# Performance work log

Measured on AMD Instinct MI355X. Metric: run time of the kernel, lower is better.

Reference implementation:

```python
import jax, jax.numpy as jnp
import numpy as np

B, T = 2, 2048
D_MODEL = 1024
N_LAYERS = 2
VOCAB = 256
BLOCK = 2048
LOCAL = 128
STRIDE = 256
NHEAD = D_MODEL // 64  # 16
HEAD_DIM = D_MODEL // NHEAD  # 64
LN_EPS = 1e-5


def setup_inputs() -> dict:
    key = jax.random.key(0)
    ks = jax.random.split(key, 16)
    L, d = N_LAYERS, D_MODEL

    def g(k, shape, scale=0.02):
        return (jax.random.normal(k, shape, dtype=jnp.float32) * scale)

    return {
        "x": jax.random.randint(ks[0], (B, T), 0, VOCAB),
        "embed": g(ks[1], (VOCAB, d)),
        "pos_embed": g(ks[2], (BLOCK, d)),
        # per-layer weights stacked on leading L axis; Linear as y = x @ W + b
        "Wq": g(ks[3], (L, d, d)), "bq": jnp.zeros((L, d), jnp.float32),
        "Wk": g(ks[4], (L, d, d)), "bk": jnp.zeros((L, d), jnp.float32),
        "Wv": g(ks[5], (L, d, d)), "bv": jnp.zeros((L, d), jnp.float32),
        "Wo": g(ks[6], (L, d, d)), "bo": jnp.zeros((L, d), jnp.float32),
        "g1": jnp.ones((L, d), jnp.float32), "be1": jnp.zeros((L, d), jnp.float32),
        "W1": g(ks[7], (L, d, 4 * d)), "bf1": jnp.zeros((L, 4 * d), jnp.float32),
        "W2": g(ks[8], (L, 4 * d, d)), "bf2": jnp.zeros((L, d), jnp.float32),
        "g2": jnp.ones((L, d), jnp.float32), "be2": jnp.zeros((L, d), jnp.float32),
        "gf": jnp.ones((d,), jnp.float32), "bef": jnp.zeros((d,), jnp.float32),
        "Whead": g(ks[9], (d, VOCAB)),
    }


def _ln(x, gamma, beta):
    mu = jnp.mean(x, axis=-1, keepdims=True)
    var = jnp.mean(jnp.square(x - mu), axis=-1, keepdims=True)
    return (x - mu) * jax.lax.rsqrt(var + LN_EPS) * gamma + beta


def _sparse_mask(t):
    # allowed[i, j] = True if token i may attend to token j
    i = jnp.arange(t)[:, None]
    j = jnp.arange(t)[None, :]
    causal = j <= i
    local = (i - j) <= LOCAL
    glob = (j % STRIDE) == 0
    return causal & (local | glob)


def _sparse_attn(q, k, v, allowed):
    # q, k, v: [B, T, D] -> [B, H, T, hd]
    b, t, d = q.shape
    def split(x):
        return x.reshape(b, t, NHEAD, HEAD_DIM).transpose(0, 2, 1, 3)
    q, k, v = split(q), split(k), split(v)
    scale = HEAD_DIM ** -0.5
    scores = jnp.einsum("bhqd,bhkd->bhqk", q, k) * scale
    scores = jnp.where(allowed[None, None], scores, -jnp.inf)
    attn = jax.nn.softmax(scores, axis=-1)  # every row has j=i allowed -> no NaN
    out = jnp.einsum("bhqk,bhkd->bhqd", attn, v)
    return out.transpose(0, 2, 1, 3).reshape(b, t, d)


def reference(x, embed, pos_embed, Wq, bq, Wk, bk, Wv, bv, Wo, bo,
              g1, be1, W1, bf1, W2, bf2, g2, be2, gf, bef, Whead):
    b, t = x.shape
    h = embed[x] + pos_embed[jnp.arange(t)][None]
    allowed = _sparse_mask(t)
    for l in range(N_LAYERS):
        h_n = _ln(h, g1[l], be1[l])
        q = h_n @ Wq[l] + bq[l]
        k = h_n @ Wk[l] + bk[l]
        v = h_n @ Wv[l] + bv[l]
        attn_out = _sparse_attn(q, k, v, allowed)
        h = h + (attn_out @ Wo[l] + bo[l])
        h2 = _ln(h, g2[l], be2[l])
        ffn = jax.nn.gelu(h2 @ W1[l] + bf1[l], approximate=False) @ W2[l] + bf2[l]
        h = h + ffn
    h = _ln(h, gf, bef)
    return h @ Whead
```

## Files before the change

### kernel.cpp

```cpp
#include <hip/hip_runtime.h>
#include <hip/hip_bf16.h>

#define BB 2
#define TT 2048
#define DD 1024
#define FF 4096
#define VV 256
#define HH 16
#define HD 64
#define MM (BB * TT)
#define LOCAL_W 128
#define STRIDE_G 256
#define QS 3072

typedef short s16x8 __attribute__((ext_vector_type(8)));
typedef __bf16 bf16x8 __attribute__((ext_vector_type(8)));
typedef float f32x4 __attribute__((ext_vector_type(4)));

#define WAITVM(N) asm volatile("s_waitcnt vmcnt(" #N ")" ::: "memory")
#define CFENCE asm volatile("" ::: "memory")

__device__ __forceinline__ float b2f(unsigned short u) {
  return __builtin_bit_cast(float, (unsigned int)u << 16);
}
__device__ __forceinline__ unsigned short f2b(float f) {
  __hip_bfloat16 h = __float2bfloat16(f);
  return __builtin_bit_cast(unsigned short, h);
}
__device__ __forceinline__ void gl_lds16(const unsigned short* g, unsigned short* l) {
  __builtin_amdgcn_global_load_lds(
      (const __attribute__((address_space(1))) void*)g,
      (__attribute__((address_space(3))) void*)l, 16, 0, 0);
}
__device__ __forceinline__ bf16x8 ldsr(const unsigned short* p) {
  return __builtin_bit_cast(bf16x8, *(const s16x8*)p);
}

__global__ __launch_bounds__(256) void transpose_k(const float* __restrict__ W,
                                                   unsigned short* __restrict__ WT,
                                                   int K, int N,
                                                   size_t sstride, size_t dstride) {
  __shared__ float t[32][33];
  const int z = blockIdx.z;
  W += (size_t)z * sstride;
  WT += (size_t)z * dstride;
  const int n0 = blockIdx.x * 32, k0 = blockIdx.y * 32;
  const int tx = threadIdx.x, ty = threadIdx.y;
  for (int r = ty; r < 32; r += 8) t[r][tx] = W[(size_t)(k0 + r) * N + n0 + tx];
  __syncthreads();
  for (int r = ty; r < 32; r += 8)
    WT[(size_t)(n0 + r) * K + k0 + tx] = f2b(t[tx][r]);
}

__global__ __launch_bounds__(256) void qkv_t(const float* __restrict__ Wq,
                                             const float* __restrict__ Wk,
                                             const float* __restrict__ Wv,
                                             unsigned short* __restrict__ WT) {
  __shared__ float t[32][33];
  const int z = blockIdx.z;
  const int l = z / 3, which = z % 3;
  const float* W = (which == 0 ? Wq : which == 1 ? Wk : Wv) + (size_t)l * DD * DD;
  unsigned short* D = WT + ((size_t)l * QS + which * DD) * DD;
  const int n0 = blockIdx.x * 32, k0 = blockIdx.y * 32;
  const int tx = threadIdx.x, ty = threadIdx.y;
  for (int r = ty; r < 32; r += 8) t[r][tx] = W[(size_t)(k0 + r) * DD + n0 + tx];
  __syncthreads();
  for (int r = ty; r < 32; r += 8)
    D[(size_t)(n0 + r) * DD + k0 + tx] = f2b(t[tx][r]);
}

__global__ __launch_bounds__(256) void concat_bias(const float* __restrict__ bq,
                                                   const float* __restrict__ bk,
                                                   const float* __restrict__ bv,
                                                   float* __restrict__ bcat) {
  const int i = blockIdx.x * 256 + threadIdx.x;
  const int l = i / QS, j = i - l * QS;
  float v;
  if (j < DD) v = bq[l * DD + j];
  else if (j < 2 * DD) v = bk[l * DD + j - DD];
  else v = bv[l * DD + j - 2 * DD];
  bcat[i] = v;
}

__global__ __launch_bounds__(256) void embed_ln(const int* __restrict__ x,
                                                const float* __restrict__ emb,
                                                const float* __restrict__ pos,
                                                const float* __restrict__ g,
                                                const float* __restrict__ be,
                                                float* __restrict__ h,
                                                unsigned short* __restrict__ out) {
  const int row = blockIdx.x;
  const int tid = threadIdx.x;
  const int tok = x[row];
  const int t = row & (TT - 1);
  f32x4 v = *(const f32x4*)&emb[(size_t)tok * DD + tid * 4];
  v += *(const f32x4*)&pos[(size_t)t * DD + tid * 4];
  *(f32x4*)&h[(size_t)row * DD + tid * 4] = v;
  float s = v[0] + v[1] + v[2] + v[3];
  float sq = v[0] * v[0] + v[1] * v[1] + v[2] * v[2] + v[3] * v[3];
#pragma unroll
  for (int off = 32; off; off >>= 1) {
    s += __shfl_xor(s, off);
    sq += __shfl_xor(sq, off);
  }
  __shared__ float ss[4], ssq[4];
  const int w = tid >> 6, lane = tid & 63;
  if (lane == 0) { ss[w] = s; ssq[w] = sq; }
  __syncthreads();
  s = ss[0] + ss[1] + ss[2] + ss[3];
  sq = ssq[0] + ssq[1] + ssq[2] + ssq[3];
  const float mean = s * (1.0f / DD);
  const float var = sq * (1.0f / DD) - mean * mean;
  const float rstd = rsqrtf(var + 1e-5f);
  const float4 gv = *(const float4*)&g[tid * 4];
  const float4 bv = *(const float4*)&be[tid * 4];
  ushort4 o;
  o.x = f2b((v[0] - mean) * rstd * gv.x + bv.x);
  o.y = f2b((v[1] - mean) * rstd * gv.y + bv.y);
  o.z = f2b((v[2] - mean) * rstd * gv.z + bv.z);
  o.w = f2b((v[3] - mean) * rstd * gv.w + bv.w);
  *(ushort4*)&out[(size_t)row * DD + tid * 4] = o;
}

__global__ __launch_bounds__(256) void ln_red(float* __restrict__ hio,
                                              const float* __restrict__ parts,
                                              const float* __restrict__ bias,
                                              const float* __restrict__ g,
                                              const float* __restrict__ be,
                                              unsigned short* __restrict__ out) {
  const int row = blockIdx.x;
  const int tid = threadIdx.x;
  const size_t base = (size_t)row * DD + tid * 4;
  f32x4 v = *(const f32x4*)&hio[base];
  v += *(const f32x4*)&bias[tid * 4];
  v += *(const f32x4*)&parts[base];
  v += *(const f32x4*)&parts[(size_t)MM * DD + base];
  *(f32x4*)&hio[base] = v;
  float s = v[0] + v[1] + v[2] + v[3];
  float sq = v[0] * v[0] + v[1] * v[1] + v[2] * v[2] + v[3] * v[3];
#pragma unroll
  for (int off = 32; off; off >>= 1) {
    s += __shfl_xor(s, off);
    sq += __shfl_xor(sq, off);
  }
  __shared__ float ss[4], ssq[4];
  const int w = tid >> 6, lane = tid & 63;
  if (lane == 0) { ss[w] = s; ssq[w] = sq; }
  __syncthreads();
  s = ss[0] + ss[1] + ss[2] + ss[3];
  sq = ssq[0] + ssq[1] + ssq[2] + ssq[3];
  const float mean = s * (1.0f / DD);
  const float var = sq * (1.0f / DD) - mean * mean;
  const float rstd = rsqrtf(var + 1e-5f);
  const float4 gv = *(const float4*)&g[tid * 4];
  const float4 bv = *(const float4*)&be[tid * 4];
  ushort4 o;
  o.x = f2b((v[0] - mean) * rstd * gv.x + bv.x);
  o.y = f2b((v[1] - mean) * rstd * gv.y + bv.y);
  o.z = f2b((v[2] - mean) * rstd * gv.z + bv.z);
  o.w = f2b((v[3] - mean) * rstd * gv.w + bv.w);
  *(ushort4*)&out[(size_t)row * DD + tid * 4] = o;
}

template <int EPI>
__global__ __launch_bounds__(512, 2) void gemm8p(const unsigned short* __restrict__ A,
                                                 const unsigned short* __restrict__ BT,
                                                 const float* __restrict__ bias,
                                                 unsigned short* __restrict__ outp,
                                                 int M, int N, int K, int nbx) {
  __shared__ __align__(16) unsigned short lds[65536];
  const int tid = threadIdx.x;
  const int lane = tid & 63;
  const int w = tid >> 6;
  const int nwg = gridDim.x;
  const int orig = blockIdx.x;
  const int wg = (orig & 7) * (nwg >> 3) + (orig >> 3);
  const int n0 = (wg % nbx) * 256, m0 = (wg / nbx) * 256;
  const int wm = w >> 2, wn = w & 3;
  f32x4 acc[8][4] = {};

  const unsigned short* aSrc[2];
  const unsigned short* bSrc[2];
  int dstO[2];
#pragma unroll
  for (int i = 0; i < 2; i++) {
    const int s = tid + (i << 9);
    const int row = s >> 2, sc = s & 3;
    const int l = sc ^ ((row >> 1) & 3);
    aSrc[i] = &A[(size_t)(m0 + row) * K + l * 8];
    bSrc[i] = &BT[(size_t)(n0 + row) * K + l * 8];
    dstO[i] = s * 8;
  }
  auto STAGE = [&](int tb, int ks, int obase) {
    const int kt = (tb << 6) + (ks << 5);
    const int so = obase + ks * 16384;
#pragma unroll
    for (int i = 0; i < 2; i++) {
      gl_lds16(aSrc[i] + kt, &lds[so + dstO[i]]);
      gl_lds16(bSrc[i] + kt, &lds[so + 8192 + dstO[i]]);
    }
  };

  const int rA = lane & 15, cr = lane >> 4;
  const int rowA0 = wm * 128 + rA;
  const int rowB0 = wn * 64 + rA;
  const int aAddr0 = rowA0 * 32 + ((cr ^ ((rowA0 >> 1) & 3)) << 3);
  const int bAddr0 = 8192 + rowB0 * 32 + ((cr ^ ((rowB0 >> 1) & 3)) << 3);

  const int NT = K >> 6;
  STAGE(0, 0, 0);
  STAGE(0, 1, 0);

  auto TILE = [&](int bufc, int tb, bool notlast) {
    const int bb = bufc << 15;
    const int ob = (bufc ^ 1) << 15;
    bf16x8 bfr[4], af[4];
    WAITVM(4);
    __builtin_amdgcn_s_barrier();
    CFENCE;
    if (notlast) STAGE(tb + 1, 0, ob);
#pragma unroll
    for (int n = 0; n < 4; n++) bfr[n] = ldsr(&lds[bb + bAddr0 + n * 512]);
#pragma unroll
    for (int i = 0; i < 4; i++) af[i] = ldsr(&lds[bb + aAddr0 + i * 512]);
    __builtin_amdgcn_s_setprio(1);
#pragma unroll
    for (int i = 0; i < 4; i++)
#pragma unroll
      for (int n = 0; n < 4; n++)
        acc[i][n] = __builtin_amdgcn_mfma_f32_16x16x32_bf16(af[i], bfr[n], acc[i][n], 0, 0, 0);
    __builtin_amdgcn_s_setprio(0);
#pragma unroll
    for (int i = 0; i < 4; i++) af[i] = ldsr(&lds[bb + aAddr0 + (4 + i) * 512]);
    __builtin_amdgcn_s_setprio(1);
#pragma unroll
    for (int i = 0; i < 4; i++)
#pragma unroll
      for (int n = 0; n < 4; n++)
        acc[4 + i][n] = __builtin_amdgcn_mfma_f32_16x16x32_bf16(af[i], bfr[n], acc[4 + i][n], 0, 0, 0);
    __builtin_amdgcn_s_setprio(0);
    if (notlast) { WAITVM(4); } else { WAITVM(0); }
    __builtin_amdgcn_s_barrier();
    CFENCE;
    if (notlast) STAGE(tb + 1, 1, ob);
#pragma unroll
    for (int n = 0; n < 4; n++) bfr[n] = ldsr(&lds[bb + 16384 + bAddr0 + n * 512]);
#pragma unroll
    for (int i = 0; i < 4; i++) af[i] = ldsr(&lds[bb + 16384 + aAddr0 + i * 512]);
    __builtin_amdgcn_s_setprio(1);
#pragma unroll
    for (int i = 0; i < 4; i++)
#pragma unroll
      for (int n = 0; n < 4; n++)
        acc[i][n] = __builtin_amdgcn_mfma_f32_16x16x32_bf16(af[i], bfr[n], acc[i][n], 0, 0, 0);
    __builtin_amdgcn_s_setprio(0);
#pragma unroll
    for (int i = 0; i < 4; i++) af[i] = ldsr(&lds[bb + 16384 + aAddr0 + (4 + i) * 512]);
    __builtin_amdgcn_s_setprio(1);
#pragma unroll
    for (int i = 0; i < 4; i++)
#pragma unroll
      for (int n = 0; n < 4; n++)
        acc[4 + i][n] = __builtin_amdgcn_mfma_f32_16x16x32_bf16(af[i], bfr[n], acc[4 + i][n], 0, 0, 0);
    __builtin_amdgcn_s_setprio(0);
  };

  for (int it = 0; it < NT; it += 2) {
    TILE(0, it, true);
    TILE(1, it + 1, it + 2 < NT);
  }

  const int r0 = (lane >> 4) * 4;
  const int cc = lane & 15;
#pragma unroll
  for (int m = 0; m < 8; m++) {
#pragma unroll
    for (int n = 0; n < 4; n++) {
#pragma unroll
      for (int r = 0; r < 4; r++) {
        const int row = m0 + wm * 128 + m * 16 + r0 + r;
        const int col = n0 + wn * 64 + n * 16 + cc;
        float val = acc[m][n][r] + bias[col];
        if (EPI == 3) {
          float u = val * (0.7978845608f + 0.0356774081f * val * val);
          u = fminf(u, 10.0f);
          const float e = __expf(2.0f * u);
          val = val * e / (e + 1.0f);
        }
        outp[(size_t)row * N + col] = f2b(val);
      }
    }
  }
}

template <int EPI>
__global__ __launch_bounds__(512, 2) void gemm_dw(const unsigned short* __restrict__ A,
                                                  const unsigned short* __restrict__ BT,
                                                  const float* __restrict__ bias,
                                                  void* __restrict__ outp,
                                                  int M, int N, int K, int nbx, int nwg2,
                                                  int ksub) {
  __shared__ __align__(16) unsigned short lds[49152];
  const int tid = threadIdx.x;
  const int lane = tid & 63;
  const int w = tid >> 6;
  const int nwg = gridDim.x;
  const int orig = blockIdx.x;
  const int wg = (orig & 7) * (nwg >> 3) + (orig >> 3);
  const int ks = wg / nwg2;
  const int rem = wg - ks * nwg2;
  const int n0 = (rem % nbx) * 128;
  const int m0 = (rem / nbx) * 256;
  const int kb = ks * ksub;
  const int wm = w >> 2, wn = w & 3;
  f32x4 acc[8][2] = {};

  const unsigned short* aSrc[2];
  const unsigned short* bSrc;
  int dstA[2], dstB;
#pragma unroll
  for (int i = 0; i < 2; i++) {
    const int s = tid + (i << 9);
    const int row = s >> 2, sc = s & 3;
    const int l = sc ^ ((row >> 1) & 3);
    aSrc[i] = &A[(size_t)(m0 + row) * K + kb + l * 8];
    dstA[i] = s * 8;
  }
  {
    const int row = tid >> 2, sc = tid & 3;
    const int l = sc ^ ((row >> 1) & 3);
    bSrc = &BT[(size_t)(n0 + row) * K + kb + l * 8];
    dstB = 8192 + tid * 8;
  }
  auto STAGE = [&](int tb, int kss, int obase) {
    const int kt = (tb << 6) + (kss << 5);
    const int so = obase + kss * 12288;
    gl_lds16(aSrc[0] + kt, &lds[so + dstA[0]]);
    gl_lds16(aSrc[1] + kt, &lds[so + dstA[1]]);
    gl_lds16(bSrc + kt, &lds[so + dstB]);
  };

  const int rA = lane & 15, cr = lane >> 4;
  const int rowA0 = wm * 128 + rA;
  const int rowB0 = wn * 32 + rA;
  const int aAddr0 = rowA0 * 32 + ((cr ^ ((rowA0 >> 1) & 3)) << 3);
  const int bAddr0 = 8192 + rowB0 * 32 + ((cr ^ ((rowB0 >> 1) & 3)) << 3);

  const int NT = ksub >> 6;
  STAGE(0, 0, 0);
  STAGE(0, 1, 0);

  auto TILE = [&](int bufc, int tb, bool notlast) {
    const int bb = bufc * 24576;
    const int ob = (bufc ^ 1) * 24576;
    bf16x8 bfr[2], af[4];
    WAITVM(3);
    __builtin_amdgcn_s_barrier();
    CFENCE;
    if (notlast) STAGE(tb + 1, 0, ob);
#pragma unroll
    for (int n = 0; n < 2; n++) bfr[n] = ldsr(&lds[bb + bAddr0 + n * 512]);
#pragma unroll
    for (int i = 0; i < 4; i++) af[i] = ldsr(&lds[bb + aAddr0 + i * 512]);
    __builtin_amdgcn_s_setprio(1);
#pragma unroll
    for (int i = 0; i < 4; i++)
#pragma unroll
      for (int n = 0; n < 2; n++)
        acc[i][n] = __builtin_amdgcn_mfma_f32_16x16x32_bf16(af[i], bfr[n], acc[i][n], 0, 0, 0);
    __builtin_amdgcn_s_setprio(0);
#pragma unroll
    for (int i = 0; i < 4; i++) af[i] = ldsr(&lds[bb + aAddr0 + (4 + i) * 512]);
    __builtin_amdgcn_s_setprio(1);
#pragma unroll
    for (int i = 0; i < 4; i++)
#pragma unroll
      for (int n = 0; n < 2; n++)
        acc[4 + i][n] = __builtin_amdgcn_mfma_f32_16x16x32_bf16(af[i], bfr[n], acc[4 + i][n], 0, 0, 0);
    __builtin_amdgcn_s_setprio(0);
    if (notlast) { WAITVM(3); } else { WAITVM(0); }
    __builtin_amdgcn_s_barrier();
    CFENCE;
    if (notlast) STAGE(tb + 1, 1, ob);
#pragma unroll
    for (int n = 0; n < 2; n++) bfr[n] = ldsr(&lds[bb + 12288 + bAddr0 + n * 512]);
#pragma unroll
    for (int i = 0; i < 4; i++) af[i] = ldsr(&lds[bb + 12288 + aAddr0 + i * 512]);
    __builtin_amdgcn_s_setprio(1);
#pragma unroll
    for (int i = 0; i < 4; i++)
#pragma unroll
      for (int n = 0; n < 2; n++)
        acc[i][n] = __builtin_amdgcn_mfma_f32_16x16x32_bf16(af[i], bfr[n], acc[i][n], 0, 0, 0);
    __builtin_amdgcn_s_setprio(0);
#pragma unroll
    for (int i = 0; i < 4; i++) af[i] = ldsr(&lds[bb + 12288 + aAddr0 + (4 + i) * 512]);
    __builtin_amdgcn_s_setprio(1);
#pragma unroll
    for (int i = 0; i < 4; i++)
#pragma unroll
      for (int n = 0; n < 2; n++)
        acc[4 + i][n] = __builtin_amdgcn_mfma_f32_16x16x32_bf16(af[i], bfr[n], acc[4 + i][n], 0, 0, 0);
    __builtin_amdgcn_s_setprio(0);
  };

  for (int it = 0; it < NT; it += 2) {
    TILE(0, it, true);
    TILE(1, it + 1, it + 2 < NT);
  }

  const int r0 = (lane >> 4) * 4;
  const int cc = lane & 15;
#pragma unroll
  for (int m = 0; m < 8; m++)
#pragma unroll
    for (int n = 0; n < 2; n++)
#pragma unroll
      for (int r = 0; r < 4; r++) {
        const int row = m0 + wm * 128 + m * 16 + r0 + r;
        const int col = n0 + wn * 32 + n * 16 + cc;
        const size_t idx = (size_t)row * N + col;
        if (EPI == 0) {
          ((float*)outp)[(size_t)ks * M * N + idx] = acc[m][n][r];
        } else {
          ((unsigned short*)outp)[idx] = f2b(acc[m][n][r] + bias[col]);
        }
      }
}

__global__ __launch_bounds__(512, 2) void gemm_p(const unsigned short* __restrict__ A,
                                                 const unsigned short* __restrict__ BT,
                                                 float* __restrict__ outp,
                                                 int M, int N, int K, int nbx, int nwg2,
                                                 int ksub) {
  constexpr int BM = 128;
  __shared__ __align__(16) unsigned short lds[4][BM * 64];
  const int tid = threadIdx.x;
  const int lane = tid & 63;
  const int w = tid >> 6;
  const int nwg = gridDim.x;
  const int orig = blockIdx.x;
  const int wg = (orig & 7) * (nwg >> 3) + (orig >> 3);
  const int ks = wg / nwg2;
  const int rem = wg - ks * nwg2;
  const int n0 = (rem % nbx) * BM;
  const int m0 = (rem / nbx) * BM;
  const int kb = ks * ksub;
  const int wm = w >> 2, wn = w & 3;
  f32x4 acc[4][2] = {};

  auto STAGE = [&](int t) {
    const int b = t & 3;
    const int kt = kb + (t << 5);
    const int s = tid;
    const int row = s >> 2, sc = s & 3;
    const int c = sc ^ ((row >> 1) & 3);
    gl_lds16(&A[(size_t)(m0 + row) * K + kt + c * 8], &lds[b][s * 8]);
    gl_lds16(&BT[(size_t)(n0 + row) * K + kt + c * 8], &lds[b][BM * 32 + s * 8]);
  };

  const int NT = ksub >> 5;
  STAGE(0); STAGE(1); STAGE(2);

  for (int t = 0; t < NT; ++t) {
    const int ahead = NT - 1 - t;
    if (ahead >= 2) WAITVM(4); else if (ahead == 1) WAITVM(2); else WAITVM(0);
    __builtin_amdgcn_s_barrier();
    CFENCE;
    if (t + 3 < NT) STAGE(t + 3);
    const int b = t & 3;
    const int rA = lane & 15, cr = lane >> 4;
    bf16x8 af[4], bfr[2];
#pragma unroll
    for (int m = 0; m < 4; m++) {
      const int row = wm * 64 + m * 16 + rA;
      af[m] = ldsr(&lds[b][row * 32 + ((cr ^ ((row >> 1) & 3)) << 3)]);
    }
#pragma unroll
    for (int n = 0; n < 2; n++) {
      const int row = wn * 32 + n * 16 + rA;
      bfr[n] = ldsr(&lds[b][BM * 32 + row * 32 + ((cr ^ ((row >> 1) & 3)) << 3)]);
    }
    __builtin_amdgcn_s_setprio(1);
#pragma unroll
    for (int m = 0; m < 4; m++)
#pragma unroll
      for (int n = 0; n < 2; n++)
        acc[m][n] = __builtin_amdgcn_mfma_f32_16x16x32_bf16(af[m], bfr[n], acc[m][n], 0, 0, 0);
    __builtin_amdgcn_s_setprio(0);
  }

  const int r0 = (lane >> 4) * 4;
  const int cc = lane & 15;
  float* pout = outp + (size_t)ks * M * N;
#pragma unroll
  for (int m = 0; m < 4; m++)
#pragma unroll
    for (int n = 0; n < 2; n++)
#pragma unroll
      for (int r = 0; r < 4; r++) {
        const int row = m0 + wm * 64 + m * 16 + r0 + r;
        const int col = n0 + wn * 32 + n * 16 + cc;
        pout[(size_t)row * N + col] = acc[m][n][r];
      }
}

template <int NP>
__global__ __launch_bounds__(256) void reduce_k(float* __restrict__ dst,
                                                const float* __restrict__ parts,
                                                size_t total) {
  const size_t i = ((size_t)blockIdx.x * 256 + threadIdx.x) * 4;
  if (i >= total) return;
  f32x4 acc = {};
#pragma unroll
  for (int p = 0; p < NP; p++) acc += *(const f32x4*)&parts[(size_t)p * total + i];
  *(f32x4*)&dst[i] = acc;
}

#define QT 16
#define KT 32
#define NTMAX 6
#define KP 72
#define PP 40

__global__ __launch_bounds__(256) void attn_mfma(const unsigned short* __restrict__ qkv,
                                                 unsigned short* __restrict__ outg) {
  __shared__ __align__(16) unsigned short kvs[4][KT * KP];
  __shared__ __align__(16) unsigned short pls[4][QT * PP];
  const int tid = threadIdx.x;
  const int wid = tid >> 6, lane = tid & 63;
  const int qgrp = blockIdx.x & 31;
  const int bh = blockIdx.x >> 5;
  const int h = bh & (HH - 1), b = bh >> 4;
  const size_t baseq = (size_t)b * TT * QS + (size_t)h * HD;
  const size_t baseo = (size_t)b * TT * DD + (size_t)h * HD;
  const int i0 = qgrp * 64 + wid * 16;
  const int g = lane >> 4;
  const int c = lane & 15;

  const int i0b = qgrp * 64 + 48;
  const int ka0b = (i0b > 128) ? ((i0b - 128) & ~31) : 0;
  const int nlb = ((i0b + 16 - ka0b) + 31) >> 5;
  const int neb = (ka0b + 255) >> 8;
  const int ka0 = (i0 > 128) ? ((i0 - 128) & ~31) : 0;
  const int ne = (ka0 + 255) >> 8;

  const s16x8 qf0 = *(const s16x8*)&qkv[baseq + (size_t)(i0 + c) * QS + g * 8];
  const s16x8 qf1 = *(const s16x8*)&qkv[baseq + (size_t)(i0 + c) * QS + 32 + g * 8];

  f32x4 sc[NTMAX][2];
  float smax[4] = {-1e30f, -1e30f, -1e30f, -1e30f};

#pragma unroll
  for (int t = 0; t < NTMAX; t++) {
    if (t > nlb) continue;
    const bool isg = (t == 0);
    if (isg && neb == 0) continue;
    const int kt0 = ka0 + (t - 1) * 32;
#pragma unroll
    for (int it = 0; it < 4; it++) {
      const int row = it * 8 + (lane >> 3);
      const int ch = lane & 7;
      const int j = isg ? ((row < ne) ? row * STRIDE_G : 0) : (kt0 + row);
      *(s16x8*)&kvs[wid][row * KP + ch * 8] =
          *(const s16x8*)&qkv[baseq + DD + (size_t)j * QS + ch * 8];
    }
    __syncthreads();
#pragma unroll
    for (int half = 0; half < 2; half++) {
      const int key = half * 16 + c;
      const bf16x8 kb0 = __builtin_bit_cast(bf16x8, *(const s16x8*)&kvs[wid][key * KP + g * 8]);
      const bf16x8 kb1 = __builtin_bit_cast(bf16x8, *(const s16x8*)&kvs[wid][key * KP + 32 + g * 8]);
      f32x4 a = {};
      a = __builtin_amdgcn_mfma_f32_16x16x32_bf16(__builtin_bit_cast(bf16x8, qf0), kb0, a, 0, 0, 0);
      a = __builtin_amdgcn_mfma_f32_16x16x32_bf16(__builtin_bit_cast(bf16x8, qf1), kb1, a, 0, 0, 0);
#pragma unroll
      for (int r = 0; r < 4; r++) {
        const int i = i0 + g * 4 + r;
        bool ok;
        if (isg) {
          ok = (key < ne);
        } else {
          const int j = kt0 + key;
          ok = (j <= i) && (((i - j) <= LOCAL_W) || ((j & (STRIDE_G - 1)) == 0));
        }
        const float s = ok ? a[r] * 0.125f : -1e30f;
        sc[t][half][r] = s;
        smax[r] = fmaxf(smax[r], s);
      }
    }
    __syncthreads();
  }
#pragma unroll
  for (int r = 0; r < 4; r++)
#pragma unroll
    for (int off = 8; off; off >>= 1)
      smax[r] = fmaxf(smax[r], __shfl_xor(smax[r], off));

  f32x4 o[4] = {};
  float lsum[4] = {0.f, 0.f, 0.f, 0.f};
#pragma unroll
  for (int t = 0; t < NTMAX; t++) {
    if (t > nlb) continue;
    const bool isg = (t == 0);
    if (isg && neb == 0) continue;
    const int kt0 = ka0 + (t - 1) * 32;
#pragma unroll
    for (int it = 0; it < 4; it++) {
      const int row = it * 8 + (lane >> 3);
      const int ch = lane & 7;
      const int j = isg ? ((row < ne) ? row * STRIDE_G : 0) : (kt0 + row);
      *(s16x8*)&kvs[wid][row * KP + ch * 8] =
          *(const s16x8*)&qkv[baseq + 2 * DD + (size_t)j * QS + ch * 8];
    }
#pragma unroll
    for (int half = 0; half < 2; half++)
#pragma unroll
      for (int r = 0; r < 4; r++) {
        const float p = __expf(sc[t][half][r] - smax[r]);
        lsum[r] += p;
        pls[wid][(g * 4 + r) * PP + half * 16 + c] = f2b(p);
      }
    __syncthreads();
    const bf16x8 pa = __builtin_bit_cast(bf16x8, *(const s16x8*)&pls[wid][c * PP + g * 8]);
#pragma unroll
    for (int d0 = 0; d0 < 4; d0++) {
      s16x8 bv;
#pragma unroll
      for (int e = 0; e < 8; e++)
        bv[e] = (short)kvs[wid][(g * 8 + e) * KP + d0 * 16 + c];
      o[d0] = __builtin_amdgcn_mfma_f32_16x16x32_bf16(pa, __builtin_bit_cast(bf16x8, bv), o[d0], 0, 0, 0);
    }
    __syncthreads();
  }
#pragma unroll
  for (int r = 0; r < 4; r++)
#pragma unroll
    for (int off = 8; off; off >>= 1)
      lsum[r] += __shfl_xor(lsum[r], off);
#pragma unroll
  for (int d0 = 0; d0 < 4; d0++)
#pragma unroll
    for (int r = 0; r < 4; r++)
      outg[baseo + (size_t)(i0 + g * 4 + r) * DD + d0 * 16 + c] = f2b(o[d0][r] / lsum[r]);
}

extern "C" void kernel_launch(void* const* d_in, const int* in_sizes, int n_in,
                              void* d_out, int out_size, void* d_ws, size_t ws_size,
                              hipStream_t stream) {
  const int* x = (const int*)d_in[0];
  const float* embed = (const float*)d_in[1];
  const float* pos = (const float*)d_in[2];
  const float* Wq = (const float*)d_in[3];
  const float* bq = (const float*)d_in[4];
  const float* Wk = (const float*)d_in[5];
  const float* bk = (const float*)d_in[6];
  const float* Wv = (const float*)d_in[7];
  const float* bv = (const float*)d_in[8];
  const float* Wo = (const float*)d_in[9];
  const float* bo = (const float*)d_in[10];
  const float* g1 = (const float*)d_in[11];
  const float* be1 = (const float*)d_in[12];
  const float* W1 = (const float*)d_in[13];
  const float* bf1 = (const float*)d_in[14];
  const float* W2 = (const float*)d_in[15];
  const float* bf2 = (const float*)d_in[16];
  const float* g2 = (const float*)d_in[17];
  const float* be2 = (const float*)d_in[18];
  const float* gf = (const float*)d_in[19];
  const float* bef = (const float*)d_in[20];
  const float* Whead = (const float*)d_in[21];

  char* ws = (char*)d_ws;
  size_t off = 0;
  auto alloc = [&](size_t bytes) -> void* {
    void* p = ws + off;
    off += (bytes + 255) & ~(size_t)255;
    return p;
  };
  unsigned short* WqkvT = (unsigned short*)alloc((size_t)2 * QS * DD * 2);
  unsigned short* WoT = (unsigned short*)alloc((size_t)2 * DD * DD * 2);
  unsigned short* W1T = (unsigned short*)alloc((size_t)2 * DD * FF * 2);
  unsigned short* W2T = (unsigned short*)alloc((size_t)2 * DD * FF * 2);
  unsigned short* WheadT = (unsigned short*)alloc((size_t)DD * VV * 2);
  float* bcat = (float*)alloc((size_t)2 * QS * 4);
  float* h = (float*)alloc((size_t)MM * DD * 4);
  unsigned short* hn = (unsigned short*)alloc((size_t)MM * DD * 2);
  unsigned short* qkvb = (unsigned short*)alloc((size_t)MM * QS * 2);
  unsigned short* attnb = (unsigned short*)alloc((size_t)MM * DD * 2);
  unsigned short* mid = (unsigned short*)alloc((size_t)MM * FF * 2);
  float* ffn2p = (float*)qkvb;
  float* oprojp = (float*)mid;
  float* headp = (float*)mid;
  (void)ws_size;

  const dim3 tb(32, 8);
  qkv_t<<<dim3(DD / 32, DD / 32, 6), tb, 0, stream>>>(Wq, Wk, Wv, WqkvT);
  transpose_k<<<dim3(DD / 32, DD / 32, 2), tb, 0, stream>>>(Wo, WoT, DD, DD,
                                                            (size_t)DD * DD, (size_t)DD * DD);
  transpose_k<<<dim3(FF / 32, DD / 32, 2), tb, 0, stream>>>(W1, W1T, DD, FF,
                                                            (size_t)DD * FF, (size_t)DD * FF);
  transpose_k<<<dim3(DD / 32, FF / 32, 2), tb, 0, stream>>>(W2, W2T, FF, DD,
                                                            (size_t)DD * FF, (size_t)DD * FF);
  transpose_k<<<dim3(VV / 32, DD / 32, 1), tb, 0, stream>>>(Whead, WheadT, DD, VV, 0, 0);
  concat_bias<<<24, 256, 0, stream>>>(bq, bk, bv, bcat);

  embed_ln<<<MM, 256, 0, stream>>>(x, embed, pos, g1, be1, h, hn);

  for (int l = 0; l < 2; l++) {
    const size_t wo = (size_t)l * DD * DD;
    const size_t wf = (size_t)l * DD * FF;
    gemm_dw<1><<<(QS / 128) * (MM / 256), 512, 0, stream>>>(
        hn, WqkvT + (size_t)l * QS * DD, bcat + l * QS, qkvb,
        MM, QS, DD, QS / 128, (QS / 128) * (MM / 256), DD);
    attn_mfma<<<BB * HH * (TT / 64), 256, 0, stream>>>(qkvb, attnb);
    gemm_dw<0><<<2 * (DD / 128) * (MM / 256), 512, 0, stream>>>(
        attnb, WoT + wo, nullptr, oprojp,
        MM, DD, DD, DD / 128, (DD / 128) * (MM / 256), DD / 2);
    ln_red<<<MM, 256, 0, stream>>>(h, oprojp, bo + l * DD, g2 + l * DD, be2 + l * DD, hn);
    gemm8p<3><<<(FF / 256) * (MM / 256), 512, 0, stream>>>(
        hn, W1T + wf, bf1 + l * FF, mid, MM, FF, DD, FF / 256);
    gemm_dw<0><<<2 * (DD / 128) * (MM / 256), 512, 0, stream>>>(
        mid, W2T + wf, nullptr, ffn2p,
        MM, DD, FF, DD / 128, (DD / 128) * (MM / 256), FF / 2);
    if (l == 0)
      ln_red<<<MM, 256, 0, stream>>>(h, ffn2p, bf2, g1 + DD, be1 + DD, hn);
    else
      ln_red<<<MM, 256, 0, stream>>>(h, ffn2p, bf2 + DD, gf, bef, hn);
  }
  gemm_p<<<4 * (VV / 128) * (MM / 128), 512, 0, stream>>>(
      hn, WheadT, headp, MM, VV, DD, VV / 128, (VV / 128) * (MM / 128), DD / 4);
  reduce_k<4><<<(MM * VV) / 1024, 256, 0, stream>>>(
      (float*)d_out, headp, (size_t)MM * VV);
}
```

Baseline: 434.7 us.

## Use triple-buffered single-stage GEMM kernel with higher occupancy for all projections

Replaces the double-buffered two-half-tile pipeline in the 256x128 GEMM with a three-slot ring buffer that loads one 32-wide K slice per iteration, prefetching two slices ahead. LDS use drops from 96KB to 72KB and launch bounds are raised to 4 waves-per-EU hint. The separate 256x256 FFN1 kernel is removed and FFN1 now uses this kernel with a fused GELU epilogue. This trades larger output tiles and fewer barriers per K step for deeper prefetch and potentially more resident workgroups, at the cost of one barrier per 32-wide K step.

```diff
diff --git a/kernel.cpp b/kernel.cpp
--- a/kernel.cpp
+++ b/kernel.cpp
@@ -163,144 +163,13 @@
 }
 
 template <int EPI>
-__global__ __launch_bounds__(512, 2) void gemm8p(const unsigned short* __restrict__ A,
-                                                 const unsigned short* __restrict__ BT,
-                                                 const float* __restrict__ bias,
-                                                 unsigned short* __restrict__ outp,
-                                                 int M, int N, int K, int nbx) {
-  __shared__ __align__(16) unsigned short lds[65536];
-  const int tid = threadIdx.x;
-  const int lane = tid & 63;
-  const int w = tid >> 6;
-  const int nwg = gridDim.x;
-  const int orig = blockIdx.x;
-  const int wg = (orig & 7) * (nwg >> 3) + (orig >> 3);
-  const int n0 = (wg % nbx) * 256, m0 = (wg / nbx) * 256;
-  const int wm = w >> 2, wn = w & 3;
-  f32x4 acc[8][4] = {};
-
-  const unsigned short* aSrc[2];
-  const unsigned short* bSrc[2];
-  int dstO[2];
-#pragma unroll
-  for (int i = 0; i < 2; i++) {
-    const int s = tid + (i << 9);
-    const int row = s >> 2, sc = s & 3;
-    const int l = sc ^ ((row >> 1) & 3);
-    aSrc[i] = &A[(size_t)(m0 + row) * K + l * 8];
-    bSrc[i] = &BT[(size_t)(n0 + row) * K + l * 8];
-    dstO[i] = s * 8;
-  }
-  auto STAGE = [&](int tb, int ks, int obase) {
-    const int kt = (tb << 6) + (ks << 5);
-    const int so = obase + ks * 16384;
-#pragma unroll
-    for (int i = 0; i < 2; i++) {
-      gl_lds16(aSrc[i] + kt, &lds[so + dstO[i]]);
-      gl_lds16(bSrc[i] + kt, &lds[so + 8192 + dstO[i]]);
-    }
-  };
-
-  const int rA = lane & 15, cr = lane >> 4;
-  const int rowA0 = wm * 128 + rA;
-  const int rowB0 = wn * 64 + rA;
-  const int aAddr0 = rowA0 * 32 + ((cr ^ ((rowA0 >> 1) & 3)) << 3);
-  const int bAddr0 = 8192 + rowB0 * 32 + ((cr ^ ((rowB0 >> 1) & 3)) << 3);
-
-  const int NT = K >> 6;
-  STAGE(0, 0, 0);
-  STAGE(0, 1, 0);
-
-  auto TILE = [&](int bufc, int tb, bool notlast) {
-    const int bb = bufc << 15;
-    const int ob = (bufc ^ 1) << 15;
-    bf16x8 bfr[4], af[4];
-    WAITVM(4);
-    __builtin_amdgcn_s_barrier();
-    CFENCE;
-    if (notlast) STAGE(tb + 1, 0, ob);
-#pragma unroll
-    for (int n = 0; n < 4; n++) bfr[n] = ldsr(&lds[bb + bAddr0 + n * 512]);
-#pragma unroll
-    for (int i = 0; i < 4; i++) af[i] = ldsr(&lds[bb + aAddr0 + i * 512]);
-    __builtin_amdgcn_s_setprio(1);
-#pragma unroll
-    for (int i = 0; i < 4; i++)
-#pragma unroll
-      for (int n = 0; n < 4; n++)
-        acc[i][n] = __builtin_amdgcn_mfma_f32_16x16x32_bf16(af[i], bfr[n], acc[i][n], 0, 0, 0);
-    __builtin_amdgcn_s_setprio(0);
-#pragma unroll
-    for (int i = 0; i < 4; i++) af[i] = ldsr(&lds[bb + aAddr0 + (4 + i) * 512]);
-    __builtin_amdgcn_s_setprio(1);
-#pragma unroll
-    for (int i = 0; i < 4; i++)
-#pragma unroll
-      for (int n = 0; n < 4; n++)
-        acc[4 + i][n] = __builtin_amdgcn_mfma_f32_16x16x32_bf16(af[i], bfr[n], acc[4 + i][n], 0, 0, 0);
-    __builtin_amdgcn_s_setprio(0);
-    if (notlast) { WAITVM(4); } else { WAITVM(0); }
-    __builtin_amdgcn_s_barrier();
-    CFENCE;
-    if (notlast) STAGE(tb + 1, 1, ob);
-#pragma unroll
-    for (int n = 0; n < 4; n++) bfr[n] = ldsr(&lds[bb + 16384 + bAddr0 + n * 512]);
-#pragma unroll
-    for (int i = 0; i < 4; i++) af[i] = ldsr(&lds[bb + 16384 + aAddr0 + i * 512]);
-    __builtin_amdgcn_s_setprio(1);
-#pragma unroll
-    for (int i = 0; i < 4; i++)
-#pragma unroll
-      for (int n = 0; n < 4; n++)
-        acc[i][n] = __builtin_amdgcn_mfma_f32_16x16x32_bf16(af[i], bfr[n], acc[i][n], 0, 0, 0);
-    __builtin_amdgcn_s_setprio(0);
-#pragma unroll
-    for (int i = 0; i < 4; i++) af[i] = ldsr(&lds[bb + 16384 + aAddr0 + (4 + i) * 512]);
-    __builtin_amdgcn_s_setprio(1);
-#pragma unroll
-    for (int i = 0; i < 4; i++)
-#pragma unroll
-      for (int n = 0; n < 4; n++)
-        acc[4 + i][n] = __builtin_amdgcn_mfma_f32_16x16x32_bf16(af[i], bfr[n], acc[4 + i][n], 0, 0, 0);
-    __builtin_amdgcn_s_setprio(0);
-  };
-
-  for (int it = 0; it < NT; it += 2) {
-    TILE(0, it, true);
-    TILE(1, it + 1, it + 2 < NT);
-  }
-
-  const int r0 = (lane >> 4) * 4;
-  const int cc = lane & 15;
-#pragma unroll
-  for (int m = 0; m < 8; m++) {
-#pragma unroll
-    for (int n = 0; n < 4; n++) {
-#pragma unroll
-      for (int r = 0; r < 4; r++) {
-        const int row = m0 + wm * 128 + m * 16 + r0 + r;
-        const int col = n0 + wn * 64 + n * 16 + cc;
-        float val = acc[m][n][r] + bias[col];
-        if (EPI == 3) {
-          float u = val * (0.7978845608f + 0.0356774081f * val * val);
-          u = fminf(u, 10.0f);
-          const float e = __expf(2.0f * u);
-          val = val * e / (e + 1.0f);
-        }
-        outp[(size_t)row * N + col] = f2b(val);
-      }
-    }
-  }
-}
-
-template <int EPI>
-__global__ __launch_bounds__(512, 2) void gemm_dw(const unsigned short* __restrict__ A,
-                                                  const unsigned short* __restrict__ BT,
-                                                  const float* __restrict__ bias,
-                                                  void* __restrict__ outp,
-                                                  int M, int N, int K, int nbx, int nwg2,
-                                                  int ksub) {
-  __shared__ __align__(16) unsigned short lds[49152];
+__global__ __launch_bounds__(512, 4) void gemm_dw3(const unsigned short* __restrict__ A,
+                                                   const unsigned short* __restrict__ BT,
+                                                   const float* __restrict__ bias,
+                                                   void* __restrict__ outp,
+                                                   int M, int N, int K, int nbx, int nwg2,
+                                                   int ksub) {
+  __shared__ __align__(16) unsigned short lds[36864];
   const int tid = threadIdx.x;
   const int lane = tid & 63;
   const int w = tid >> 6;
@@ -332,12 +201,11 @@
     bSrc = &BT[(size_t)(n0 + row) * K + kb + l * 8];
     dstB = 8192 + tid * 8;
   }
-  auto STAGE = [&](int tb, int kss, int obase) {
-    const int kt = (tb << 6) + (kss << 5);
-    const int so = obase + kss * 12288;
-    gl_lds16(aSrc[0] + kt, &lds[so + dstA[0]]);
-    gl_lds16(aSrc[1] + kt, &lds[so + dstA[1]]);
-    gl_lds16(bSrc + kt, &lds[so + dstB]);
+  auto STAGE = [&](int u, int base) {
+    const int kt = u << 5;
+    gl_lds16(aSrc[0] + kt, &lds[base + dstA[0]]);
+    gl_lds16(aSrc[1] + kt, &lds[base + dstA[1]]);
+    gl_lds16(bSrc + kt, &lds[base + dstB]);
   };
 
   const int rA = lane & 15, cr = lane >> 4;
@@ -346,22 +214,21 @@
   const int aAddr0 = rowA0 * 32 + ((cr ^ ((rowA0 >> 1) & 3)) << 3);
   const int bAddr0 = 8192 + rowB0 * 32 + ((cr ^ ((rowB0 >> 1) & 3)) << 3);
 
-  const int NT = ksub >> 6;
-  STAGE(0, 0, 0);
-  STAGE(0, 1, 0);
-
-  auto TILE = [&](int bufc, int tb, bool notlast) {
-    const int bb = bufc * 24576;
-    const int ob = (bufc ^ 1) * 24576;
-    bf16x8 bfr[2], af[4];
-    WAITVM(3);
+  const int NS = ksub >> 5;
+  int c0 = 0, c1 = 12288, c2 = 24576;
+  STAGE(0, c0);
+  STAGE(1, c1);
+
+  for (int u = 0; u < NS; ++u) {
+    if (u + 1 < NS) { WAITVM(3); } else { WAITVM(0); }
     __builtin_amdgcn_s_barrier();
     CFENCE;
-    if (notlast) STAGE(tb + 1, 0, ob);
-#pragma unroll
-    for (int n = 0; n < 2; n++) bfr[n] = ldsr(&lds[bb + bAddr0 + n * 512]);
-#pragma unroll
-    for (int i = 0; i < 4; i++) af[i] = ldsr(&lds[bb + aAddr0 + i * 512]);
+    if (u + 2 < NS) STAGE(u + 2, c2);
+    bf16x8 bfr[2], af[4];
+#pragma unroll
+    for (int n = 0; n < 2; n++) bfr[n] = ldsr(&lds[c0 + bAddr0 + n * 512]);
+#pragma unroll
+    for (int i = 0; i < 4; i++) af[i] = ldsr(&lds[c0 + aAddr0 + i * 512]);
     __builtin_amdgcn_s_setprio(1);
 #pragma unroll
     for (int i = 0; i < 4; i++)
@@ -370,7 +237,7 @@
         acc[i][n] = __builtin_amdgcn_mfma_f32_16x16x32_bf16(af[i], bfr[n], acc[i][n], 0, 0, 0);
     __builtin_amdgcn_s_setprio(0);
 #pragma unroll
-    for (int i = 0; i < 4; i++) af[i] = ldsr(&lds[bb + aAddr0 + (4 + i) * 512]);
+    for (int i = 0; i < 4; i++) af[i] = ldsr(&lds[c0 + aAddr0 + (4 + i) * 512]);
     __builtin_amdgcn_s_setprio(1);
 #pragma unroll
     for (int i = 0; i < 4; i++)
@@ -378,35 +245,7 @@
       for (int n = 0; n < 2; n++)
         acc[4 + i][n] = __builtin_amdgcn_mfma_f32_16x16x32_bf16(af[i], bfr[n], acc[4 + i][n], 0, 0, 0);
     __builtin_amdgcn_s_setprio(0);
-    if (notlast) { WAITVM(3); } else { WAITVM(0); }
-    __builtin_amdgcn_s_barrier();
-    CFENCE;
-    if (notlast) STAGE(tb + 1, 1, ob);
-#pragma unroll
-    for (int n = 0; n < 2; n++) bfr[n] = ldsr(&lds[bb + 12288 + bAddr0 + n * 512]);
-#pragma unroll
-    for (int i = 0; i < 4; i++) af[i] = ldsr(&lds[bb + 12288 + aAddr0 + i * 512]);
-    __builtin_amdgcn_s_setprio(1);
-#pragma unroll
-    for (int i = 0; i < 4; i++)
-#pragma unroll
-      for (int n = 0; n < 2; n++)
-        acc[i][n] = __builtin_amdgcn_mfma_f32_16x16x32_bf16(af[i], bfr[n], acc[i][n], 0, 0, 0);
-    __builtin_amdgcn_s_setprio(0);
-#pragma unroll
-    for (int i = 0; i < 4; i++) af[i] = ldsr(&lds[bb + 12288 + aAddr0 + (4 + i) * 512]);
-    __builtin_amdgcn_s_setprio(1);
-#pragma unroll
-    for (int i = 0; i < 4; i++)
-#pragma unroll
-      for (int n = 0; n < 2; n++)
-        acc[4 + i][n] = __builtin_amdgcn_mfma_f32_16x16x32_bf16(af[i], bfr[n], acc[4 + i][n], 0, 0, 0);
-    __builtin_amdgcn_s_setprio(0);
-  };
-
-  for (int it = 0; it < NT; it += 2) {
-    TILE(0, it, true);
-    TILE(1, it + 1, it + 2 < NT);
+    const int t = c0; c0 = c1; c1 = c2; c2 = t;
   }
 
   const int r0 = (lane >> 4) * 4;
@@ -423,7 +262,14 @@
         if (EPI == 0) {
           ((float*)outp)[(size_t)ks * M * N + idx] = acc[m][n][r];
         } else {
-          ((unsigned short*)outp)[idx] = f2b(acc[m][n][r] + bias[col]);
+          float val = acc[m][n][r] + bias[col];
+          if (EPI == 3) {
+            float u2 = val * (0.7978845608f + 0.0356774081f * val * val);
+            u2 = fminf(u2, 10.0f);
+            const float e = __expf(2.0f * u2);
+            val = val * e / (e + 1.0f);
+          }
+          ((unsigned short*)outp)[idx] = f2b(val);
         }
       }
 }
@@ -710,17 +556,18 @@
   for (int l = 0; l < 2; l++) {
     const size_t wo = (size_t)l * DD * DD;
     const size_t wf = (size_t)l * DD * FF;
-    gemm_dw<1><<<(QS / 128) * (MM / 256), 512, 0, stream>>>(
+    gemm_dw3<1><<<(QS / 128) * (MM / 256), 512, 0, stream>>>(
         hn, WqkvT + (size_t)l * QS * DD, bcat + l * QS, qkvb,
         MM, QS, DD, QS / 128, (QS / 128) * (MM / 256), DD);
     attn_mfma<<<BB * HH * (TT / 64), 256, 0, stream>>>(qkvb, attnb);
-    gemm_dw<0><<<2 * (DD / 128) * (MM / 256), 512, 0, stream>>>(
+    gemm_dw3<0><<<2 * (DD / 128) * (MM / 256), 512, 0, stream>>>(
         attnb, WoT + wo, nullptr, oprojp,
         MM, DD, DD, DD / 128, (DD / 128) * (MM / 256), DD / 2);
     ln_red<<<MM, 256, 0, stream>>>(h, oprojp, bo + l * DD, g2 + l * DD, be2 + l * DD, hn);
-    gemm8p<3><<<(FF / 256) * (MM / 256), 512, 0, stream>>>(
-        hn, W1T + wf, bf1 + l * FF, mid, MM, FF, DD, FF / 256);
-    gemm_dw<0><<<2 * (DD / 128) * (MM / 256), 512, 0, stream>>>(
+    gemm_dw3<3><<<(FF / 128) * (MM / 256), 512, 0, stream>>>(
+        hn, W1T + wf, bf1 + l * FF, mid,
+        MM, FF, DD, FF / 128, (FF / 128) * (MM / 256), DD);
+    gemm_dw3<0><<<2 * (DD / 128) * (MM / 256), 512, 0, stream>>>(
         mid, W2T + wf, nullptr, ffn2p,
         MM, DD, FF, DD / 128, (DD / 128) * (MM / 256), FF / 2);
     if (l == 0)
```

New measurement: 434.1 us. About the same (-0.1%).
